# Kernel optimization log

Measured on AMD Instinct MI355X. Metric: run time of the kernel, lower is better.

Reference implementation:

```python
import jax, jax.numpy as jnp
import numpy as np

EPS = 1e-5

def _ln(x, g=None, b=None):
    m = jnp.mean(x, axis=-1, keepdims=True)
    v = jnp.var(x, axis=-1, keepdims=True)
    y = (x - m) / jnp.sqrt(v + EPS)
    if g is not None:
        y = y * g + b
    return y

def setup_inputs() -> dict:
    key = jax.random.key(0)
    B, N, C = 2, 2048, 1024   # batch, tokens, query_dim
    H, D = 16, 64             # heads, dim_head -> inner = 1024
    inner = H * D
    ks = jax.random.split(key, 8)
    s = C ** -0.5
    inp = {
        'x':   jax.random.normal(ks[0], (B, N, C), jnp.float32),
        'w_q': jax.random.normal(ks[1], (C, inner), jnp.float32) * s,
        'b_q': jnp.zeros((inner,), jnp.float32),
        'w_k': jax.random.normal(ks[2], (C, inner), jnp.float32) * s,
        'b_k': jnp.zeros((inner,), jnp.float32),
        'w_v': jax.random.normal(ks[3], (C, inner), jnp.float32) * s,
        'b_v': jnp.zeros((inner,), jnp.float32),
        'g_q': jnp.ones((inner,), jnp.float32),
        'be_q': jnp.zeros((inner,), jnp.float32),
        'g_k': jnp.ones((inner,), jnp.float32),
        'be_k': jnp.zeros((inner,), jnp.float32),
        # to_out is zero-initialized in the torch code; use small random weights
        # so forward/backward are non-trivial for correctness testing.
        'w_o': jax.random.normal(ks[4], (inner, C), jnp.float32) * s,
        'b_o': jnp.zeros((C,), jnp.float32),
    }
    return inp

def reference(x, w_q, b_q, w_k, b_k, w_v, b_v, g_q, be_q, g_k, be_k, w_o, b_o):
    B, N, C = x.shape
    inner = w_q.shape[1]
    H = 16
    D = inner // H
    xn = _ln(x)                                  # pre-norm, no affine
    ctx = xn                                     # self-attention (context=None)
    silu = jax.nn.silu
    q = silu(xn) @ w_q + b_q                     # [B,N,inner]
    k = silu(ctx) @ w_k + b_k
    v = silu(ctx) @ w_v + b_v
    q = _ln(q, g_q, be_q)
    k = _ln(k, g_k, be_k)
    q = q * (inner ** -0.5)                      # NB: scale by inner_dim, pre-split
    q = q.reshape(B, N, H, D)
    k = k.reshape(B, N, H, D)
    v = v.reshape(B, N, H, D)
    w = jnp.einsum('bihd,bjhd->bhij', q, k)      # [B,H,N,N]
    w = jax.nn.softmax(w, axis=-1)
    o = jnp.einsum('bhij,bjhd->bihd', w, v).reshape(B, N, inner)
    return silu(o) @ w_o + b_o
```

## Files before the change

### kernel.cpp

```cpp
#include <hip/hip_runtime.h>
#include <hip/hip_bf16.h>
#include <math.h>

#define LN_EPS 1e-5f

typedef __attribute__((ext_vector_type(8))) short bf16x8;
typedef __attribute__((ext_vector_type(8))) short short8;
typedef __attribute__((ext_vector_type(4))) float f32x4;
typedef unsigned short ushort_t;

__device__ __forceinline__ float silu_f(float x) {
    return x / (1.0f + __expf(-x));
}

__device__ __forceinline__ ushort_t f2bf(float f) {
    __hip_bfloat16 h = __float2bfloat16(f);
    return *reinterpret_cast<ushort_t*>(&h);
}

__device__ __forceinline__ float bf2f(ushort_t u) {
    __hip_bfloat16 h = *reinterpret_cast<__hip_bfloat16*>(&u);
    return __bfloat162float(h);
}

__device__ __forceinline__ unsigned pk2(float a, float b) {
    unsigned r;
    asm("v_cvt_pk_bf16_f32 %0, %1, %2" : "=v"(r) : "v"(a), "v"(b));
    return r;
}

__device__ __forceinline__ float fast_exp2(float x) {
#if defined(__has_builtin)
#if __has_builtin(__builtin_amdgcn_exp2f)
    return __builtin_amdgcn_exp2f(x);
#else
    return exp2f(x);
#endif
#else
    return exp2f(x);
#endif
}

__device__ __forceinline__ void gld16(const void* g, void* lds) {
    __builtin_amdgcn_global_load_lds(
        (const __attribute__((address_space(1))) unsigned int*)g,
        (__attribute__((address_space(3))) unsigned int*)lds, 16, 0, 0);
}

__device__ __forceinline__ float2 block_reduce2(float2 p, float2* sbuf) {
    #pragma unroll
    for (int off = 32; off > 0; off >>= 1) {
        p.x += __shfl_down(p.x, off, 64);
        p.y += __shfl_down(p.y, off, 64);
    }
    int lane = threadIdx.x & 63;
    int wid  = threadIdx.x >> 6;
    if (lane == 0) sbuf[wid] = p;
    __syncthreads();
    if (threadIdx.x == 0) {
        float2 r = sbuf[0];
        for (int i = 1; i < 4; ++i) { r.x += sbuf[i].x; r.y += sbuf[i].y; }
        sbuf[0] = r;
    }
    __syncthreads();
    return sbuf[0];
}

__global__ __launch_bounds__(256) void ln_silu_kernel(
    const float* __restrict__ x, ushort_t* __restrict__ out)
{
    __shared__ float2 sbuf[4];
    const int C = 1024;
    int row = blockIdx.x;
    const float4* xr = (const float4*)(x + (size_t)row * C);
    float4 v = xr[threadIdx.x];
    float2 p;
    p.x = v.x + v.y + v.z + v.w;
    p.y = v.x*v.x + v.y*v.y + v.z*v.z + v.w*v.w;
    float2 s = block_reduce2(p, sbuf);
    float mean = s.x / (float)C;
    float var  = s.y / (float)C - mean * mean;
    float rstd = rsqrtf(var + LN_EPS);
    ushort4 y;
    y.x = f2bf(silu_f((v.x - mean) * rstd));
    y.y = f2bf(silu_f((v.y - mean) * rstd));
    y.z = f2bf(silu_f((v.z - mean) * rstd));
    y.w = f2bf(silu_f((v.w - mean) * rstd));
    ((ushort4*)(out + (size_t)row * C))[threadIdx.x] = y;
}

__global__ __launch_bounds__(256) void ln_affine_bf16(
    ushort_t* __restrict__ qk0, ushort_t* __restrict__ qk1,
    const float* __restrict__ g0, const float* __restrict__ be0,
    const float* __restrict__ g1, const float* __restrict__ be1,
    float scale0, float scale1)
{
    __shared__ float2 sbuf[4];
    const int C = 1024;
    int which = blockIdx.y;
    ushort_t* q = which ? qk1 : qk0;
    const float* g  = which ? g1  : g0;
    const float* be = which ? be1 : be0;
    float scale = which ? scale1 : scale0;
    int row = blockIdx.x;
    ushort4 u = ((ushort4*)(q + (size_t)row * C))[threadIdx.x];
    float v0 = bf2f(u.x), v1 = bf2f(u.y), v2 = bf2f(u.z), v3 = bf2f(u.w);
    float2 p;
    p.x = v0 + v1 + v2 + v3;
    p.y = v0*v0 + v1*v1 + v2*v2 + v3*v3;
    float2 s = block_reduce2(p, sbuf);
    float mean = s.x / (float)C;
    float var  = s.y / (float)C - mean * mean;
    float rstd = rsqrtf(var + LN_EPS);
    float4 gv = ((const float4*)g)[threadIdx.x];
    float4 bv = ((const float4*)be)[threadIdx.x];
    ushort4 y;
    y.x = f2bf(((v0 - mean) * rstd * gv.x + bv.x) * scale);
    y.y = f2bf(((v1 - mean) * rstd * gv.y + bv.y) * scale);
    y.z = f2bf(((v2 - mean) * rstd * gv.z + bv.z) * scale);
    y.w = f2bf(((v3 - mean) * rstd * gv.w + bv.w) * scale);
    ((ushort4*)(q + (size_t)row * C))[threadIdx.x] = y;
}

struct W4 { const float* p[4]; };

__global__ __launch_bounds__(256) void transpose_w(W4 w, ushort_t* __restrict__ outbase)
{
    __shared__ float Ls[64][65];
    int z = blockIdx.z;
    const float* in = w.p[z];
    ushort_t* out = outbase + (size_t)z * 1024 * 1024;
    int r0 = blockIdx.y * 64, c0 = blockIdx.x * 64;
    int t = threadIdx.x, r = t >> 2, j = (t & 3) * 16;
    #pragma unroll
    for (int i = 0; i < 4; ++i) {
        float4 v = *(const float4*)(in + (size_t)(r0 + r) * 1024 + c0 + j + i * 4);
        Ls[r][j + i*4 + 0] = v.x;
        Ls[r][j + i*4 + 1] = v.y;
        Ls[r][j + i*4 + 2] = v.z;
        Ls[r][j + i*4 + 3] = v.w;
    }
    __syncthreads();
    __align__(16) ushort_t tmp[16];
    #pragma unroll
    for (int i = 0; i < 16; ++i) tmp[i] = f2bf(Ls[j + i][r]);
    ushort_t* op = out + (size_t)(c0 + r) * 1024 + r0 + j;
    *(short8*)(op)     = *(short8*)(tmp);
    *(short8*)(op + 8) = *(short8*)(tmp + 8);
}

template<int BM, bool OUT_BF16>
__global__ __launch_bounds__(256) void gemm_mfma(
    const ushort_t* __restrict__ A, const ushort_t* __restrict__ Bt0,
    const float* __restrict__ b0, const float* __restrict__ b1,
    const float* __restrict__ b2, void* __restrict__ out0,
    ushort_t* __restrict__ vt_out,
    int M, int N, int K)
{
    constexpr int BK = 64;
    constexpr int MI = BM / 32;
    __shared__ ushort_t Smem[2 * (BM + 128) * BK];
    ushort_t* As0 = Smem;
    ushort_t* Bs0 = Smem + BM * BK;
    ushort_t* As1 = Smem + (BM + 128) * BK;
    ushort_t* Bs1 = As1 + BM * BK;

    constexpr int NY = (BM == 128) ? 32 : 64;
    constexpr int NZ = (BM == 128) ? 3 : 1;
    constexpr int NB = 8 * NY * NZ;
    constexpr int CHUNK = NB / 8;
    int lin = blockIdx.x + 8 * (blockIdx.y + NY * blockIdx.z);
    int swz = (lin & 7) * CHUNK + (lin >> 3);
    int bx = swz & 7;
    int by = (swz >> 3) & (NY - 1);
    int z  = swz / (8 * NY);

    const ushort_t* Bt = Bt0 + (size_t)z * N * K;
    const float* bias = (z == 0) ? b0 : (z == 1) ? b1 : b2;

    int t = threadIdx.x;
    int lane = t & 63, wv = t >> 6;
    int wr = wv >> 1, wc = wv & 1;
    int quad = lane >> 4, ln16 = lane & 15;

    int row0 = by * BM;
    int col0 = bx * 128;

    const f32x4 zero4 = {0.f, 0.f, 0.f, 0.f};
    f32x4 acc[MI][4];
    #pragma unroll
    for (int i = 0; i < MI; ++i)
        #pragma unroll
        for (int j = 0; j < 4; ++j) acc[i][j] = zero4;

    auto stage = [&](ushort_t* AsB, ushort_t* BsB, int kt) {
        #pragma unroll
        for (int c = 0; c < BM / 32; ++c) {
            int idx = c * 256 + t;
            int r = idx >> 3, ch = idx & 7;
            int g = ch ^ (r & 7);
            gld16(A + (size_t)(row0 + r) * K + kt + g * 8,
                  AsB + (size_t)(c * 256 + wv * 64) * 8);
        }
        #pragma unroll
        for (int c = 0; c < 4; ++c) {
            int idx = c * 256 + t;
            int r = idx >> 3, ch = idx & 7;
            int g = ch ^ (r & 7);
            gld16(Bt + (size_t)(col0 + r) * K + kt + g * 8,
                  BsB + (size_t)(c * 256 + wv * 64) * 8);
        }
    };

    auto compute = [&](const ushort_t* AsB, const ushort_t* BsB) {
        #pragma unroll
        for (int s = 0; s < 2; ++s) {
            bf16x8 af[MI], bf[4];
            int g = s * 4 + quad;
            #pragma unroll
            for (int i = 0; i < MI; ++i) {
                int m = wr * (BM / 2) + i * 16 + ln16;
                af[i] = *(const bf16x8*)(AsB + (size_t)(m * 8 + (g ^ (m & 7))) * 8);
            }
            #pragma unroll
            for (int j = 0; j < 4; ++j) {
                int n = wc * 64 + j * 16 + ln16;
                bf[j] = *(const bf16x8*)(BsB + (size_t)(n * 8 + (g ^ (n & 7))) * 8);
            }
            __builtin_amdgcn_s_setprio(1);
            #pragma unroll
            for (int i = 0; i < MI; ++i)
                #pragma unroll
                for (int j = 0; j < 4; ++j)
                    acc[i][j] = __builtin_amdgcn_mfma_f32_16x16x32_bf16(
                        af[i], bf[j], acc[i][j], 0, 0, 0);
            __builtin_amdgcn_s_setprio(0);
        }
    };

    auto wait_prev = [&]() {
        if constexpr (BM == 128) asm volatile("s_waitcnt vmcnt(8)" ::: "memory");
        else                     asm volatile("s_waitcnt vmcnt(6)" ::: "memory");
    };

    const int NTk = K / BK;
    stage(As0, Bs0, 0);
    #pragma unroll 1
    for (int it = 0; it < NTk; it += 2) {
        stage(As1, Bs1, (it + 1) * BK);
        wait_prev();
        __builtin_amdgcn_s_barrier();
        __builtin_amdgcn_sched_barrier(0);
        compute(As0, Bs0);
        __builtin_amdgcn_sched_barrier(0);
        __builtin_amdgcn_s_barrier();

        if (it + 2 < NTk) {
            stage(As0, Bs0, (it + 2) * BK);
            wait_prev();
        } else {
            asm volatile("s_waitcnt vmcnt(0)" ::: "memory");
        }
        __builtin_amdgcn_s_barrier();
        __builtin_amdgcn_sched_barrier(0);
        compute(As1, Bs1);
        __builtin_amdgcn_sched_barrier(0);
        __builtin_amdgcn_s_barrier();
    }

    if (OUT_BF16 && z == 2 && BM == 128) {
        ushort_t* tb = Smem + wv * 4096;
        int tok0 = row0 + wr * 64;
        int chn0 = col0 + wc * 64;
        #pragma unroll
        for (int j = 0; j < 4; ++j) {
            int chl = j * 16 + ln16;
            float bv = bias[chn0 + chl];
            #pragma unroll
            for (int i = 0; i < MI; ++i) {
                uint2 uu;
                uu.x = pk2(acc[i][j][0] + bv, acc[i][j][1] + bv);
                uu.y = pk2(acc[i][j][2] + bv, acc[i][j][3] + bv);
                int hc = i * 4 + quad;
                int phys = hc ^ ((chl & 7) << 1);
                *(uint2*)(tb + chl * 64 + phys * 4) = uu;
            }
        }
        int bb2 = tok0 >> 11;
        int tokb = tok0 & 2047;
        #pragma unroll
        for (int p = 0; p < 8; ++p) {
            int chl = p * 8 + (lane >> 3);
            int tc  = lane & 7;
            int ptc = tc ^ (chl & 7);
            uint4 vvv = *(const uint4*)(tb + chl * 64 + ptc * 8);
            *(uint4*)(vt_out + ((size_t)bb2 * 1024 + chn0 + chl) * 2048 + tokb + tc * 8) = vvv;
        }
    } else {
        #pragma unroll
        for (int j = 0; j < 4; ++j) {
            int col = col0 + wc * 64 + j * 16 + ln16;
            float bv = bias[col];
            #pragma unroll
            for (int i = 0; i < MI; ++i) {
                int rowb = row0 + wr * (BM / 2) + i * 16 + quad * 4;
                #pragma unroll
                for (int r = 0; r < 4; ++r) {
                    float val = acc[i][j][r] + bv;
                    if (OUT_BF16) {
                        ushort_t* out = (ushort_t*)out0 + (size_t)z * M * N;
                        out[(size_t)(rowb + r) * N + col] = f2bf(val);
                    } else {
                        float* out = (float*)out0;
                        out[(size_t)(rowb + r) * N + col] = val;
                    }
                }
            }
        }
    }
}

__global__ __launch_bounds__(256, 4) void flash_mfma(
    const ushort_t* __restrict__ qb, const ushort_t* __restrict__ kb,
    const ushort_t* __restrict__ vT, ushort_t* __restrict__ ob)
{
    const int N = 2048, HD = 1024, D = 64, H = 16;
    const int KT = 64;
    const int NT = N / KT;
    __shared__ ushort_t Ks[2][64 * 64];
    __shared__ ushort_t Vs[2][64 * 64];

    int t = threadIdx.x, lane = t & 63, wv = t >> 6;
    int quad = lane >> 4, ln16 = lane & 15;
    int lin = blockIdx.x + 32 * (blockIdx.y + 16 * blockIdx.z);
    int swz = ((lin & 7) << 7) + (lin >> 3);
    int qt = swz & 31, h = (swz >> 5) & 15, b = swz >> 9;

    size_t qk_base = (size_t)b * N * HD + (size_t)h * D;
    size_t vt_base = (size_t)(b * H + h) * D * N;

    bf16x8 qf[2];
    {
        const ushort_t* qp = qb + qk_base + (size_t)(qt * 64 + wv * 16 + ln16) * HD;
        qf[0] = *(const bf16x8*)(qp + quad * 8);
        qf[1] = *(const bf16x8*)(qp + 32 + quad * 8);
    }

    bf16x8 ones;
    #pragma unroll
    for (int i = 0; i < 8; ++i) ones[i] = (short)0x3F80;

    const f32x4 zero4 = {0.f, 0.f, 0.f, 0.f};
    f32x4 oacc[4];
    f32x4 lacc = zero4;
    #pragma unroll
    for (int j = 0; j < 4; ++j) oacc[j] = zero4;

    auto stage_K = [&](ushort_t* KsB, int kt) {
        #pragma unroll
        for (int c = 0; c < 2; ++c) {
            int idx = c * 256 + t;
            int r = idx >> 3, ch = idx & 7, g = ch ^ (r & 7);
            int pr = (r & ~31) | (((r >> 2) & 3) << 3) | (((r >> 4) & 1) << 2) | (r & 3);
            gld16(kb + qk_base + (size_t)(kt + pr) * HD + g * 8,
                  KsB + (size_t)(c * 256 + wv * 64) * 8);
        }
    };
    auto stage_V = [&](ushort_t* VsB, int kt) {
        #pragma unroll
        for (int c = 0; c < 2; ++c) {
            int idx = c * 256 + t;
            int r = idx >> 3, ch = idx & 7, g = ch ^ (r & 7);
            gld16(vT + vt_base + (size_t)r * N + kt + g * 8,
                  VsB + (size_t)(c * 256 + wv * 64) * 8);
        }
    };

    auto qk_tile = [&](const ushort_t* KsB, f32x4 (&st)[4]) {
        __builtin_amdgcn_s_setprio(1);
        #pragma unroll
        for (int j = 0; j < 4; ++j) {
            int n = j * 16 + ln16;
            bf16x8 kf0 = *(const bf16x8*)(KsB + ((size_t)n * 8 + (quad       ^ (n & 7))) * 8);
            st[j] = __builtin_amdgcn_mfma_f32_16x16x32_bf16(kf0, qf[0], zero4, 0, 0, 0);
        }
        #pragma unroll
        for (int j = 0; j < 4; ++j) {
            int n = j * 16 + ln16;
            bf16x8 kf1 = *(const bf16x8*)(KsB + ((size_t)n * 8 + ((4 + quad) ^ (n & 7))) * 8);
            st[j] = __builtin_amdgcn_mfma_f32_16x16x32_bf16(kf1, qf[1], st[j], 0, 0, 0);
        }
        __builtin_amdgcn_s_setprio(0);
    };

    auto sm_pv = [&](f32x4 (&st)[4], const ushort_t* VsB) {
        bf16x8 vf[2][4];
        #pragma unroll
        for (int w = 0; w < 2; ++w) {
            int phys = (w * 4 + quad) ^ (ln16 & 7);
            #pragma unroll
            for (int mt = 0; mt < 4; ++mt)
                vf[w][mt] = *(const bf16x8*)(VsB + (size_t)(mt * 16 + ln16) * 64 + phys * 8);
        }
        #pragma unroll
        for (int j = 0; j < 4; ++j) {
            st[j][0] = fast_exp2(st[j][0]);
            st[j][1] = fast_exp2(st[j][1]);
            st[j][2] = fast_exp2(st[j][2]);
            st[j][3] = fast_exp2(st[j][3]);
        }
        #pragma unroll
        for (int w = 0; w < 2; ++w) {
            uint4 up;
            up.x = pk2(st[2*w][0],   st[2*w][1]);
            up.y = pk2(st[2*w][2],   st[2*w][3]);
            up.z = pk2(st[2*w+1][0], st[2*w+1][1]);
            up.w = pk2(st[2*w+1][2], st[2*w+1][3]);
            bf16x8 pf = __builtin_bit_cast(bf16x8, up);
            __builtin_amdgcn_s_setprio(1);
            lacc = __builtin_amdgcn_mfma_f32_16x16x32_bf16(ones, pf, lacc, 0, 0, 0);
            #pragma unroll
            for (int mt = 0; mt < 4; ++mt)
                oacc[mt] = __builtin_amdgcn_mfma_f32_16x16x32_bf16(vf[w][mt], pf, oacc[mt], 0, 0, 0);
            __builtin_amdgcn_s_setprio(0);
        }
    };

    f32x4 stA[4], stB[4];

    stage_K(Ks[0], 0);       stage_V(Vs[0], 0);
    stage_K(Ks[1], KT);      stage_V(Vs[1], KT);
    asm volatile("s_waitcnt vmcnt(4)" ::: "memory");
    __builtin_amdgcn_s_barrier();
    __builtin_amdgcn_sched_barrier(0);
    qk_tile(Ks[0], stA);
    __builtin_amdgcn_sched_barrier(0);
    __builtin_amdgcn_s_barrier();

    #pragma unroll 1
    for (int it = 0; it < NT - 2; it += 2) {
        stage_K(Ks[0], (it + 2) * KT);
        asm volatile("s_waitcnt vmcnt(4)" ::: "memory");
        __builtin_amdgcn_s_barrier();
        __builtin_amdgcn_sched_barrier(0);
        qk_tile(Ks[1], stB);
        sm_pv(stA, Vs[0]);
        __builtin_amdgcn_sched_barrier(0);
        __builtin_amdgcn_s_barrier();
        stage_V(Vs[0], (it + 2) * KT);

        stage_K(Ks[1], (it + 3) * KT);
        asm volatile("s_waitcnt vmcnt(4)" ::: "memory");
        __builtin_amdgcn_s_barrier();
        __builtin_amdgcn_sched_barrier(0);
        qk_tile(Ks[0], stA);
        sm_pv(stB, Vs[1]);
        __builtin_amdgcn_sched_barrier(0);
        __builtin_amdgcn_s_barrier();
        stage_V(Vs[1], (it + 3) * KT);
    }

    asm volatile("s_waitcnt vmcnt(2)" ::: "memory");
    __builtin_amdgcn_s_barrier();
    __builtin_amdgcn_sched_barrier(0);
    qk_tile(Ks[1], stB);
    sm_pv(stA, Vs[0]);
    asm volatile("s_waitcnt vmcnt(0)" ::: "memory");
    __builtin_amdgcn_s_barrier();
    __builtin_amdgcn_sched_barrier(0);
    sm_pv(stB, Vs[1]);

    float inv = 1.0f / lacc[0];
    size_t rowoff = qk_base + (size_t)(qt * 64 + wv * 16 + ln16) * HD;
    #pragma unroll
    for (int mt = 0; mt < 4; ++mt) {
        float o0 = silu_f(oacc[mt][0] * inv);
        float o1 = silu_f(oacc[mt][1] * inv);
        float o2 = silu_f(oacc[mt][2] * inv);
        float o3 = silu_f(oacc[mt][3] * inv);
        uint2 uu;
        uu.x = pk2(o0, o1);
        uu.y = pk2(o2, o3);
        *(uint2*)(ob + rowoff + mt * 16 + quad * 4) = uu;
    }
}

extern "C" void kernel_launch(void* const* d_in, const int* in_sizes, int n_in,
                              void* d_out, int out_size, void* d_ws, size_t ws_size,
                              hipStream_t stream) {
    const float* x    = (const float*)d_in[0];
    const float* w_q  = (const float*)d_in[1];
    const float* b_q  = (const float*)d_in[2];
    const float* w_k  = (const float*)d_in[3];
    const float* b_k  = (const float*)d_in[4];
    const float* w_v  = (const float*)d_in[5];
    const float* b_v  = (const float*)d_in[6];
    const float* g_q  = (const float*)d_in[7];
    const float* be_q = (const float*)d_in[8];
    const float* g_k  = (const float*)d_in[9];
    const float* be_k = (const float*)d_in[10];
    const float* w_o  = (const float*)d_in[11];
    const float* b_o  = (const float*)d_in[12];
    float* out = (float*)d_out;

    const int B = 2, N = 2048, C = 1024, H = 16, INNER = 1024;
    const int M = B * N;
    const size_t MC = (size_t)M * C;

    ushort_t* ws  = (ushort_t*)d_ws;
    ushort_t* sx  = ws;
    ushort_t* qkv = ws + MC;
    ushort_t* vTp = ws + 4 * MC;
    ushort_t* wT  = ws + 5 * MC;

    ushort_t* qbuf = qkv;
    ushort_t* kbuf = qkv + MC;
    ushort_t* obuf = sx;

    W4 w4; w4.p[0] = w_q; w4.p[1] = w_k; w4.p[2] = w_v; w4.p[3] = w_o;
    transpose_w<<<dim3(16, 16, 4), 256, 0, stream>>>(w4, wT);

    ln_silu_kernel<<<M, 256, 0, stream>>>(x, sx);

    gemm_mfma<128, true><<<dim3(INNER / 128, M / 128, 3), 256, 0, stream>>>(
        sx, wT, b_q, b_k, b_v, qkv, vTp, M, INNER, C);

    ln_affine_bf16<<<dim3(M, 2), 256, 0, stream>>>(
        qbuf, kbuf, g_q, be_q, g_k, be_k, 0.03125f * 1.44269504f, 1.0f);

    flash_mfma<<<dim3(N / 64, H, B), 256, 0, stream>>>(qbuf, kbuf, vTp, obuf);

    gemm_mfma<64, false><<<dim3(C / 128, M / 64, 1), 256, 0, stream>>>(
        obuf, wT + (size_t)3 * 1024 * 1024, b_o, b_o, b_o, out, nullptr, M, C, INNER);
}
```

Measured before the change: 199.5 us.

## Split flash attention waves 2x2 over query rows and key halves with LDS reduction

```diff
diff --git a/kernel.cpp b/kernel.cpp
--- a/kernel.cpp
+++ b/kernel.cpp
@@ -332,6 +332,7 @@
 
     int t = threadIdx.x, lane = t & 63, wv = t >> 6;
     int quad = lane >> 4, ln16 = lane & 15;
+    int qh = wv & 1, kh = wv >> 1;
     int lin = blockIdx.x + 32 * (blockIdx.y + 16 * blockIdx.z);
     int swz = ((lin & 7) << 7) + (lin >> 3);
     int qt = swz & 31, h = (swz >> 5) & 15, b = swz >> 9;
@@ -339,11 +340,15 @@
     size_t qk_base = (size_t)b * N * HD + (size_t)h * D;
     size_t vt_base = (size_t)(b * H + h) * D * N;
 
-    bf16x8 qf[2];
+    bf16x8 qf0a, qf0b, qf1a, qf1b;
     {
-        const ushort_t* qp = qb + qk_base + (size_t)(qt * 64 + wv * 16 + ln16) * HD;
-        qf[0] = *(const bf16x8*)(qp + quad * 8);
-        qf[1] = *(const bf16x8*)(qp + 32 + quad * 8);
+        const ushort_t* qp0 = qb + qk_base +
+            (size_t)(qt * 64 + qh * 32 + ln16) * HD;
+        qf0a = *(const bf16x8*)(qp0 + quad * 8);
+        qf0b = *(const bf16x8*)(qp0 + 32 + quad * 8);
+        const ushort_t* qp1 = qp0 + (size_t)16 * HD;
+        qf1a = *(const bf16x8*)(qp1 + quad * 8);
+        qf1b = *(const bf16x8*)(qp1 + 32 + quad * 8);
     }
 
     bf16x8 ones;
@@ -351,10 +356,9 @@
     for (int i = 0; i < 8; ++i) ones[i] = (short)0x3F80;
 
     const f32x4 zero4 = {0.f, 0.f, 0.f, 0.f};
-    f32x4 oacc[4];
-    f32x4 lacc = zero4;
-    #pragma unroll
-    for (int j = 0; j < 4; ++j) oacc[j] = zero4;
+    f32x4 o00 = zero4, o01 = zero4, o02 = zero4, o03 = zero4;
+    f32x4 o10 = zero4, o11 = zero4, o12 = zero4, o13 = zero4;
+    f32x4 lac0 = zero4, lac1 = zero4;
 
     auto stage_K = [&](ushort_t* KsB, int kt) {
         #pragma unroll
@@ -376,64 +380,76 @@
         }
     };
 
-    auto qk_tile = [&](const ushort_t* KsB, f32x4 (&st)[4]) {
+    auto qk_tile = [&](const ushort_t* KsB,
+                       f32x4& s0q0, f32x4& s0q1, f32x4& s1q0, f32x4& s1q1) {
+        int n0 = kh * 32 + ln16;
+        int n1 = n0 + 16;
         __builtin_amdgcn_s_setprio(1);
-        #pragma unroll
-        for (int j = 0; j < 4; ++j) {
-            int n = j * 16 + ln16;
-            bf16x8 kf0 = *(const bf16x8*)(KsB + ((size_t)n * 8 + (quad       ^ (n & 7))) * 8);
-            st[j] = __builtin_amdgcn_mfma_f32_16x16x32_bf16(kf0, qf[0], zero4, 0, 0, 0);
-        }
-        #pragma unroll
-        for (int j = 0; j < 4; ++j) {
-            int n = j * 16 + ln16;
-            bf16x8 kf1 = *(const bf16x8*)(KsB + ((size_t)n * 8 + ((4 + quad) ^ (n & 7))) * 8);
-            st[j] = __builtin_amdgcn_mfma_f32_16x16x32_bf16(kf1, qf[1], st[j], 0, 0, 0);
+        {
+            bf16x8 kf0 = *(const bf16x8*)(KsB + ((size_t)n0 * 8 + (quad ^ (n0 & 7))) * 8);
+            bf16x8 kf1 = *(const bf16x8*)(KsB + ((size_t)n1 * 8 + (quad ^ (n1 & 7))) * 8);
+            s0q0 = __builtin_amdgcn_mfma_f32_16x16x32_bf16(kf0, qf0a, zero4, 0, 0, 0);
+            s0q1 = __builtin_amdgcn_mfma_f32_16x16x32_bf16(kf0, qf1a, zero4, 0, 0, 0);
+            s1q0 = __builtin_amdgcn_mfma_f32_16x16x32_bf16(kf1, qf0a, zero4, 0, 0, 0);
+            s1q1 = __builtin_amdgcn_mfma_f32_16x16x32_bf16(kf1, qf1a, zero4, 0, 0, 0);
+        }
+        {
+            int g = 4 + quad;
+            bf16x8 kf0 = *(const bf16x8*)(KsB + ((size_t)n0 * 8 + (g ^ (n0 & 7))) * 8);
+            bf16x8 kf1 = *(const bf16x8*)(KsB + ((size_t)n1 * 8 + (g ^ (n1 & 7))) * 8);
+            s0q0 = __builtin_amdgcn_mfma_f32_16x16x32_bf16(kf0, qf0b, s0q0, 0, 0, 0);
+            s0q1 = __builtin_amdgcn_mfma_f32_16x16x32_bf16(kf0, qf1b, s0q1, 0, 0, 0);
+            s1q0 = __builtin_amdgcn_mfma_f32_16x16x32_bf16(kf1, qf0b, s1q0, 0, 0, 0);
+            s1q1 = __builtin_amdgcn_mfma_f32_16x16x32_bf16(kf1, qf1b, s1q1, 0, 0, 0);
         }
         __builtin_amdgcn_s_setprio(0);
     };
 
-    auto sm_pv = [&](f32x4 (&st)[4], const ushort_t* VsB) {
-        bf16x8 vf[2][4];
-        #pragma unroll
-        for (int w = 0; w < 2; ++w) {
-            int phys = (w * 4 + quad) ^ (ln16 & 7);
-            #pragma unroll
-            for (int mt = 0; mt < 4; ++mt)
-                vf[w][mt] = *(const bf16x8*)(VsB + (size_t)(mt * 16 + ln16) * 64 + phys * 8);
-        }
-        #pragma unroll
-        for (int j = 0; j < 4; ++j) {
-            st[j][0] = fast_exp2(st[j][0]);
-            st[j][1] = fast_exp2(st[j][1]);
-            st[j][2] = fast_exp2(st[j][2]);
-            st[j][3] = fast_exp2(st[j][3]);
-        }
-        #pragma unroll
-        for (int w = 0; w < 2; ++w) {
-            uint4 up;
-            up.x = pk2(st[2*w][0],   st[2*w][1]);
-            up.y = pk2(st[2*w][2],   st[2*w][3]);
-            up.z = pk2(st[2*w+1][0], st[2*w+1][1]);
-            up.w = pk2(st[2*w+1][2], st[2*w+1][3]);
-            bf16x8 pf = __builtin_bit_cast(bf16x8, up);
-            __builtin_amdgcn_s_setprio(1);
-            lacc = __builtin_amdgcn_mfma_f32_16x16x32_bf16(ones, pf, lacc, 0, 0, 0);
-            #pragma unroll
-            for (int mt = 0; mt < 4; ++mt)
-                oacc[mt] = __builtin_amdgcn_mfma_f32_16x16x32_bf16(vf[w][mt], pf, oacc[mt], 0, 0, 0);
-            __builtin_amdgcn_s_setprio(0);
-        }
-    };
-
-    f32x4 stA[4], stB[4];
+    auto sm_pv = [&](f32x4& s0q0, f32x4& s0q1, f32x4& s1q0, f32x4& s1q1,
+                     const ushort_t* VsB) {
+        int phys = (kh * 4 + quad) ^ (ln16 & 7);
+        bf16x8 vf0 = *(const bf16x8*)(VsB + (size_t)(ln16)      * 64 + phys * 8);
+        bf16x8 vf1 = *(const bf16x8*)(VsB + (size_t)(16 + ln16) * 64 + phys * 8);
+        bf16x8 vf2 = *(const bf16x8*)(VsB + (size_t)(32 + ln16) * 64 + phys * 8);
+        bf16x8 vf3 = *(const bf16x8*)(VsB + (size_t)(48 + ln16) * 64 + phys * 8);
+        s0q0[0] = fast_exp2(s0q0[0]); s0q0[1] = fast_exp2(s0q0[1]);
+        s0q0[2] = fast_exp2(s0q0[2]); s0q0[3] = fast_exp2(s0q0[3]);
+        s0q1[0] = fast_exp2(s0q1[0]); s0q1[1] = fast_exp2(s0q1[1]);
+        s0q1[2] = fast_exp2(s0q1[2]); s0q1[3] = fast_exp2(s0q1[3]);
+        s1q0[0] = fast_exp2(s1q0[0]); s1q0[1] = fast_exp2(s1q0[1]);
+        s1q0[2] = fast_exp2(s1q0[2]); s1q0[3] = fast_exp2(s1q0[3]);
+        s1q1[0] = fast_exp2(s1q1[0]); s1q1[1] = fast_exp2(s1q1[1]);
+        s1q1[2] = fast_exp2(s1q1[2]); s1q1[3] = fast_exp2(s1q1[3]);
+        uint4 up0, up1;
+        up0.x = pk2(s0q0[0], s0q0[1]); up0.y = pk2(s0q0[2], s0q0[3]);
+        up0.z = pk2(s1q0[0], s1q0[1]); up0.w = pk2(s1q0[2], s1q0[3]);
+        up1.x = pk2(s0q1[0], s0q1[1]); up1.y = pk2(s0q1[2], s0q1[3]);
+        up1.z = pk2(s1q1[0], s1q1[1]); up1.w = pk2(s1q1[2], s1q1[3]);
+        bf16x8 pf0 = __builtin_bit_cast(bf16x8, up0);
+        bf16x8 pf1 = __builtin_bit_cast(bf16x8, up1);
+        __builtin_amdgcn_s_setprio(1);
+        lac0 = __builtin_amdgcn_mfma_f32_16x16x32_bf16(ones, pf0, lac0, 0, 0, 0);
+        lac1 = __builtin_amdgcn_mfma_f32_16x16x32_bf16(ones, pf1, lac1, 0, 0, 0);
+        o00 = __builtin_amdgcn_mfma_f32_16x16x32_bf16(vf0, pf0, o00, 0, 0, 0);
+        o10 = __builtin_amdgcn_mfma_f32_16x16x32_bf16(vf0, pf1, o10, 0, 0, 0);
+        o01 = __builtin_amdgcn_mfma_f32_16x16x32_bf16(vf1, pf0, o01, 0, 0, 0);
+        o11 = __builtin_amdgcn_mfma_f32_16x16x32_bf16(vf1, pf1, o11, 0, 0, 0);
+        o02 = __builtin_amdgcn_mfma_f32_16x16x32_bf16(vf2, pf0, o02, 0, 0, 0);
+        o12 = __builtin_amdgcn_mfma_f32_16x16x32_bf16(vf2, pf1, o12, 0, 0, 0);
+        o03 = __builtin_amdgcn_mfma_f32_16x16x32_bf16(vf3, pf0, o03, 0, 0, 0);
+        o13 = __builtin_amdgcn_mfma_f32_16x16x32_bf16(vf3, pf1, o13, 0, 0, 0);
+        __builtin_amdgcn_s_setprio(0);
+    };
+
+    f32x4 sA0q0, sA0q1, sA1q0, sA1q1;
+    f32x4 sB0q0, sB0q1, sB1q0, sB1q1;
 
     stage_K(Ks[0], 0);       stage_V(Vs[0], 0);
     stage_K(Ks[1], KT);      stage_V(Vs[1], KT);
     asm volatile("s_waitcnt vmcnt(4)" ::: "memory");
     __builtin_amdgcn_s_barrier();
     __builtin_amdgcn_sched_barrier(0);
-    qk_tile(Ks[0], stA);
+    qk_tile(Ks[0], sA0q0, sA0q1, sA1q0, sA1q1);
     __builtin_amdgcn_sched_barrier(0);
     __builtin_amdgcn_s_barrier();
 
@@ -443,8 +459,8 @@
         asm volatile("s_waitcnt vmcnt(4)" ::: "memory");
         __builtin_amdgcn_s_barrier();
         __builtin_amdgcn_sched_barrier(0);
-        qk_tile(Ks[1], stB);
-        sm_pv(stA, Vs[0]);
+        qk_tile(Ks[1], sB0q0, sB0q1, sB1q0, sB1q1);
+        sm_pv(sA0q0, sA0q1, sA1q0, sA1q1, Vs[0]);
         __builtin_amdgcn_sched_barrier(0);
         __builtin_amdgcn_s_barrier();
         stage_V(Vs[0], (it + 2) * KT);
@@ -453,8 +469,8 @@
         asm volatile("s_waitcnt vmcnt(4)" ::: "memory");
         __builtin_amdgcn_s_barrier();
         __builtin_amdgcn_sched_barrier(0);
-        qk_tile(Ks[0], stA);
-        sm_pv(stB, Vs[1]);
+        qk_tile(Ks[0], sA0q0, sA0q1, sA1q0, sA1q1);
+        sm_pv(sB0q0, sB0q1, sB1q0, sB1q1, Vs[1]);
         __builtin_amdgcn_sched_barrier(0);
         __builtin_amdgcn_s_barrier();
         stage_V(Vs[1], (it + 3) * KT);
@@ -463,25 +479,61 @@
     asm volatile("s_waitcnt vmcnt(2)" ::: "memory");
     __builtin_amdgcn_s_barrier();
     __builtin_amdgcn_sched_barrier(0);
-    qk_tile(Ks[1], stB);
-    sm_pv(stA, Vs[0]);
+    qk_tile(Ks[1], sB0q0, sB0q1, sB1q0, sB1q1);
+    sm_pv(sA0q0, sA0q1, sA1q0, sA1q1, Vs[0]);
     asm volatile("s_waitcnt vmcnt(0)" ::: "memory");
     __builtin_amdgcn_s_barrier();
     __builtin_amdgcn_sched_barrier(0);
-    sm_pv(stB, Vs[1]);
-
-    float inv = 1.0f / lacc[0];
-    size_t rowoff = qk_base + (size_t)(qt * 64 + wv * 16 + ln16) * HD;
-    #pragma unroll
-    for (int mt = 0; mt < 4; ++mt) {
-        float o0 = silu_f(oacc[mt][0] * inv);
-        float o1 = silu_f(oacc[mt][1] * inv);
-        float o2 = silu_f(oacc[mt][2] * inv);
-        float o3 = silu_f(oacc[mt][3] * inv);
-        uint2 uu;
-        uu.x = pk2(o0, o1);
-        uu.y = pk2(o2, o3);
-        *(uint2*)(ob + rowoff + mt * 16 + quad * 4) = uu;
+    sm_pv(sB0q0, sB0q1, sB1q0, sB1q1, Vs[1]);
+
+    __syncthreads();
+    float* obufL = (float*)Ks;
+    float* lbufL = (float*)Vs;
+    if (kh == 1) {
+        int r0 = (qh * 2 + 0) * 4;
+        *(f32x4*)(obufL + ((r0 + 0) * 64 + lane) * 4) = o00;
+        *(f32x4*)(obufL + ((r0 + 1) * 64 + lane) * 4) = o01;
+        *(f32x4*)(obufL + ((r0 + 2) * 64 + lane) * 4) = o02;
+        *(f32x4*)(obufL + ((r0 + 3) * 64 + lane) * 4) = o03;
+        int r1 = (qh * 2 + 1) * 4;
+        *(f32x4*)(obufL + ((r1 + 0) * 64 + lane) * 4) = o10;
+        *(f32x4*)(obufL + ((r1 + 1) * 64 + lane) * 4) = o11;
+        *(f32x4*)(obufL + ((r1 + 2) * 64 + lane) * 4) = o12;
+        *(f32x4*)(obufL + ((r1 + 3) * 64 + lane) * 4) = o13;
+        lbufL[(qh * 2 + 0) * 64 + lane] = lac0[0];
+        lbufL[(qh * 2 + 1) * 64 + lane] = lac1[0];
+    }
+    __syncthreads();
+    if (kh == 0) {
+        size_t rowoff0 = qk_base + (size_t)(qt * 64 + qh * 32 + ln16) * HD;
+        #define FIN(OV, MT, RG, ROFF, LINV) { \
+            f32x4 p = *(const f32x4*)(obufL + (((RG) + (MT)) * 64 + lane) * 4); \
+            float f0 = silu_f((OV[0] + p[0]) * (LINV)); \
+            float f1 = silu_f((OV[1] + p[1]) * (LINV)); \
+            float f2 = silu_f((OV[2] + p[2]) * (LINV)); \
+            float f3 = silu_f((OV[3] + p[3]) * (LINV)); \
+            uint2 uu; uu.x = pk2(f0, f1); uu.y = pk2(f2, f3); \
+            *(uint2*)(ob + (ROFF) + (MT) * 16 + quad * 4) = uu; }
+        {
+            float l = lac0[0] + lbufL[(qh * 2 + 0) * 64 + lane];
+            float inv = 1.0f / l;
+            int r0 = (qh * 2 + 0) * 4;
+            FIN(o00, 0, r0, rowoff0, inv);
+            FIN(o01, 1, r0, rowoff0, inv);
+            FIN(o02, 2, r0, rowoff0, inv);
+            FIN(o03, 3, r0, rowoff0, inv);
+        }
+        {
+            float l = lac1[0] + lbufL[(qh * 2 + 1) * 64 + lane];
+            float inv = 1.0f / l;
+            int r1 = (qh * 2 + 1) * 4;
+            size_t rowoff1 = rowoff0 + (size_t)16 * HD;
+            FIN(o10, 0, r1, rowoff1, inv);
+            FIN(o11, 1, r1, rowoff1, inv);
+            FIN(o12, 2, r1, rowoff1, inv);
+            FIN(o13, 3, r1, rowoff1, inv);
+        }
+        #undef FIN
     }
 }
 
```

New measurement: 270.2 us. 1.35x slower.
